# Kernel optimization log

Measured on AMD Instinct MI355X. Metric: run time of the kernel, lower is better.

## Reference

```python
import jax, jax.numpy as jnp
import numpy as np

N = 50000    # num_nodes
E = 800000   # num_edges
IN = 256     # input_dim
H = 256      # hidden_dim
EPS = 1e-5   # BatchNorm eps


def setup_inputs() -> dict:
    key = jax.random.key(0)
    ks = jax.random.split(key, 12)
    def nrm(k, shp, s=0.05):
        return jax.random.normal(k, shp, dtype=jnp.float32) * s
    return {
        "x": jax.random.normal(ks[0], (N, IN), dtype=jnp.float32),
        "edge_index": jax.random.randint(ks[1], (2, E), 0, N, dtype=jnp.int32),
        "edge_weight": jax.random.uniform(ks[2], (E,), dtype=jnp.float32),
        # GCNConv 1 / 2 (PyG stores weight as [in, out]; bias [out])
        "W1": nrm(ks[3], (IN, H)), "b1": jnp.zeros((H,), jnp.float32),
        "W2": nrm(ks[4], (H, H)), "b2": jnp.zeros((H,), jnp.float32),
        # BatchNorm1d 1 / 2
        "gamma1": jnp.ones((H,), jnp.float32), "beta1": jnp.zeros((H,), jnp.float32),
        "gamma2": jnp.ones((H,), jnp.float32), "beta2": jnp.zeros((H,), jnp.float32),
        # LSTM 1 (input 2H) and LSTM 2 (input H), PyTorch gate order i,f,g,o
        "Wih1": nrm(ks[5], (4 * H, 2 * H)), "Whh1": nrm(ks[6], (4 * H, H)),
        "bih1": jnp.zeros((4 * H,), jnp.float32), "bhh1": jnp.zeros((4 * H,), jnp.float32),
        "Wih2": nrm(ks[7], (4 * H, H)), "Whh2": nrm(ks[8], (4 * H, H)),
        "bih2": jnp.zeros((4 * H,), jnp.float32), "bhh2": jnp.zeros((4 * H,), jnp.float32),
    }


def reference(x, edge_index, edge_weight, W1, b1, W2, b2, gamma1, beta1,
              gamma2, beta2, Wih1, Whh1, bih1, bhh1, Wih2, Whh2, bih2, bhh2):
    src, dst = edge_index[0], edge_index[1]
    # GCN symmetric normalization with added self-loops (fill value 1.0)
    loops = jnp.arange(N, dtype=src.dtype)
    src_a = jnp.concatenate([src, loops])
    dst_a = jnp.concatenate([dst, loops])
    ew_a = jnp.concatenate([edge_weight, jnp.ones((N,), edge_weight.dtype)])
    deg = jax.ops.segment_sum(ew_a, dst_a, num_segments=N)
    deg_safe = jnp.where(deg > 0, deg, 1.0)
    dinv = jnp.where(deg > 0, jax.lax.rsqrt(deg_safe), 0.0)
    norm = dinv[src_a] * ew_a * dinv[dst_a]  # [E+N]

    def gcn(h, W, b):
        m = (h @ W)[src_a] * norm[:, None]               # gather + scale messages
        return jax.ops.segment_sum(m, dst_a, num_segments=N) + b

    def bn(h, g, bta):  # training-mode BatchNorm1d (batch stats, biased var)
        mu = jnp.mean(h, axis=0)
        var = jnp.mean((h - mu) ** 2, axis=0)
        return (h - mu) * jax.lax.rsqrt(var + EPS) * g + bta

    def lstm_step0(inp, Wih, bih, bhh):  # single step from h0=c0=0 (window=1)
        gates = inp @ Wih.T + bih + bhh  # Whh term vanishes since h0=0
        i, f, g, o = jnp.split(gates, 4, axis=-1)
        c = jax.nn.sigmoid(i) * jnp.tanh(g)  # f*c0 = 0
        return jax.nn.sigmoid(o) * jnp.tanh(c)

    h1 = bn(jax.nn.relu(gcn(x, W1, b1)), gamma1, beta1)   # [N, H]
    h2 = bn(jax.nn.relu(gcn(h1, W2, b2)), gamma2, beta2)  # [N, H]
    Xc = jnp.concatenate([h1, h2], axis=1)                # [N, 2H]
    hL1 = lstm_step0(Xc, Wih1, bih1, bhh1)                # LSTM1 final hidden
    hL2 = lstm_step0(hL1, Wih2, bih2, bhh2)               # LSTM2 final hidden
    # S with window=1 reduces to x itself
    return jnp.concatenate([hL1, hL2, x], axis=1)         # [N, 2H + IN]
```

## Files before the change

### kernel.cpp

```cpp
#include <hip/hip_runtime.h>
#include <math.h>

#define NN 50000
#define NE 800000

typedef __attribute__((ext_vector_type(8))) short bf8;
typedef __attribute__((ext_vector_type(4))) float f32x4;
typedef unsigned int u32;

__device__ __forceinline__ unsigned short f2b(float f){
  union{float f;unsigned u;} v; v.f=f;
  unsigned r=v.u+0x7fff+((v.u>>16)&1u);
  return (unsigned short)(r>>16);
}
__device__ __forceinline__ float b2f(unsigned short h){
  union{unsigned u;float f;} v; v.u=((unsigned)h)<<16; return v.f;
}
__device__ __forceinline__ float fsigm(float x){ return __builtin_amdgcn_rcpf(1.f+__expf(-x)); }
__device__ __forceinline__ float ftanh(float x){ return 1.f-2.f*__builtin_amdgcn_rcpf(__expf(2.f*x)+1.f); }

__device__ __forceinline__ void gload16(const unsigned short* g, unsigned short* l){
  __builtin_amdgcn_global_load_lds((const __attribute__((address_space(1))) u32*)g,
                                   (__attribute__((address_space(3))) u32*)l,
                                   16,0,0);
}

__global__ __launch_bounds__(256) void k_init(float* deg,int* cnt,float* colsum,float* colsq){
  int i=blockIdx.x*256+threadIdx.x;
  if(i<NN){deg[i]=1.0f;cnt[i]=0;}
  if(i<256){colsum[i]=0.f;colsq[i]=0.f;}
}

__global__ __launch_bounds__(256) void k_deg(const int* __restrict__ ei,const float* __restrict__ ew,
                                             float* deg,int* cnt){
  int e=blockIdx.x*256+threadIdx.x;
  if(e<NE){int d=ei[NE+e];atomicAdd(&deg[d],ew[e]);atomicAdd(&cnt[d],1);}
}

__global__ __launch_bounds__(256) void k_dinv(const float* __restrict__ deg,float* dinv){
  int i=blockIdx.x*256+threadIdx.x;
  if(i<NN){float d=deg[i];dinv[i]=d>0.f?rsqrtf(d):0.f;}
}

__global__ __launch_bounds__(1024) void k_scan(const int* __restrict__ cnt,int* row_ptr,int* cursor){
  __shared__ int s[1024];
  __shared__ int carry;
  int tid=threadIdx.x;
  if(tid==0)carry=0;
  __syncthreads();
  for(int base=0;base<NN;base+=1024){
    int i=base+tid;
    int v=(i<NN)?cnt[i]:0;
    s[tid]=v;__syncthreads();
    for(int off=1;off<1024;off<<=1){
      int t=(tid>=off)?s[tid-off]:0;
      __syncthreads();
      s[tid]+=t;__syncthreads();
    }
    int excl=carry+s[tid]-v;
    if(i<NN){row_ptr[i]=excl;cursor[i]=excl;}
    __syncthreads();
    if(tid==1023)carry+=s[1023];
    __syncthreads();
  }
  if(tid==0)row_ptr[NN]=carry;
}

__global__ __launch_bounds__(256) void k_scatter(const int* __restrict__ ei,const float* __restrict__ ew,
    const float* __restrict__ dinv,int* cursor,int* csr_src,float* csr_w){
  int e=blockIdx.x*256+threadIdx.x;
  if(e<NE){
    int s=ei[e],d=ei[NE+e];
    float wv=dinv[s]*ew[e]*dinv[d];
    int p=atomicAdd(&cursor[d],1);
    csr_src[p]=s;csr_w[p]=wv;
  }
}

__global__ __launch_bounds__(256) void k_wt(const float* __restrict__ W,unsigned short* __restrict__ Wt){
  int j=blockIdx.x,k=threadIdx.x;
  Wt[j*256+k]=f2b(W[k*256+j]);
}
__global__ __launch_bounds__(256) void k_f2b(const float* __restrict__ s,unsigned short* __restrict__ d,int n){
  int i=blockIdx.x*256+threadIdx.x;
  if(i<n)d[i]=f2b(s[i]);
}
__global__ __launch_bounds__(256) void k_cast(const float* __restrict__ s,unsigned short* __restrict__ d){
  long i=(long)blockIdx.x*256+threadIdx.x;
  float4 v=*(const float4*)&s[i*4];
  ushort4 o;o.x=f2b(v.x);o.y=f2b(v.y);o.z=f2b(v.z);o.w=f2b(v.w);
  *(ushort4*)&d[i*4]=o;
}
__global__ __launch_bounds__(256) void k_bsum(const float* __restrict__ a,const float* __restrict__ b,
                                              float* __restrict__ s,int n){
  int i=blockIdx.x*256+threadIdx.x;
  if(i<n)s[i]=a[i]+b[i];
}

__global__ __launch_bounds__(256,2) void k_gemm_mfma(
    const unsigned short* __restrict__ A,int lda,const unsigned short* __restrict__ Bt,int K,
    unsigned short* __restrict__ Cb){
  __shared__ unsigned short As[2][4096];
  __shared__ unsigned short Bs[2][4096];
  int tid=threadIdx.x;
  int row0=blockIdx.x*128,col0=blockIdx.y*128;
  int lane=tid&63,l15=lane&15,quad=lane>>4;
  int wid=tid>>6,wm=wid>>1,wn=wid&1;
  int sr=tid>>2;
  int aoff=((tid&3)^((tid>>3)&3))*8;
  int xq=quad^((l15>>1)&3);
  long ar0=row0+sr;    if(ar0>=NN)ar0=NN-1;
  long ar1=row0+64+sr; if(ar1>=NN)ar1=NN-1;
  const unsigned short* a0p=A+ar0*lda+aoff;
  const unsigned short* a1p=A+ar1*lda+aoff;
  const unsigned short* b0p=Bt+(long)(col0+sr)*K+aoff;
  const unsigned short* b1p=Bt+(long)(col0+64+sr)*K+aoff;
  int lb=wid*512;
  f32x4 acc[4][4]={};
  int nt=K/32;
  gload16(a0p,&As[0][lb]); gload16(a1p,&As[0][2048+lb]);
  gload16(b0p,&Bs[0][lb]); gload16(b1p,&Bs[0][2048+lb]);
  __syncthreads();
  for(int t=0;t<nt;t++){
    int cur=t&1;
    if(t+1<nt){
      int k0=(t+1)*32;int nxt=cur^1;
      gload16(a0p+k0,&As[nxt][lb]); gload16(a1p+k0,&As[nxt][2048+lb]);
      gload16(b0p+k0,&Bs[nxt][lb]); gload16(b1p+k0,&Bs[nxt][2048+lb]);
    }
    bf8 af[4],bfg[4];
    #pragma unroll
    for(int i=0;i<4;i++){
      af[i] =*(const bf8*)&As[cur][(wm*64+i*16+l15)*32+xq*8];
      bfg[i]=*(const bf8*)&Bs[cur][(wn*64+i*16+l15)*32+xq*8];
    }
    #pragma unroll
    for(int mi=0;mi<4;mi++)
      #pragma unroll
      for(int ni=0;ni<4;ni++)
        acc[mi][ni]=__builtin_amdgcn_mfma_f32_16x16x32_bf16(af[mi],bfg[ni],acc[mi][ni],0,0,0);
    __syncthreads();
  }
  #pragma unroll
  for(int mi=0;mi<4;mi++){
    #pragma unroll
    for(int r=0;r<4;r++){
      int node=row0+wm*64+mi*16+quad*4+r;
      if(node>=NN)continue;
      #pragma unroll
      for(int ni=0;ni<4;ni++){
        int col=col0+wn*64+ni*16+l15;
        Cb[(long)node*256+col]=f2b(acc[mi][ni][r]);
      }
    }
  }
}

__global__ __launch_bounds__(256,2) void k_lstm_mfma(
    const unsigned short* __restrict__ A,int lda,int K,
    const unsigned short* __restrict__ Wb,const float* __restrict__ bsum,
    float* __restrict__ Hout,int ldh,unsigned short* __restrict__ Hb){
  __shared__ unsigned short As[2][4096];
  __shared__ unsigned short Bs[2][6144];
  int tid=threadIdx.x;
  int row0=blockIdx.x*128,m0=blockIdx.y*64;
  int lane=tid&63,l15=lane&15,quad=lane>>4;
  int wid=tid>>6,wm=wid>>1,wn=wid&1;
  int sr=tid>>2;
  int aoff=((tid&3)^((tid>>3)&3))*8;
  int xq=quad^((l15>>1)&3);
  long ar0=row0+sr;    if(ar0>=NN)ar0=NN-1;
  long ar1=row0+64+sr; if(ar1>=NN)ar1=NN-1;
  const unsigned short* a0p=A+ar0*lda+aoff;
  const unsigned short* a1p=A+ar1*lda+aoff;
  const unsigned short* wip=Wb+(long)(    m0+sr)*K+aoff;
  const unsigned short* wgp=Wb+(long)(512+m0+sr)*K+aoff;
  const unsigned short* wop=Wb+(long)(768+m0+sr)*K+aoff;
  int lb=wid*512;
  f32x4 ai[4][2]={},ag[4][2]={},ao[4][2]={};
  int nt=K/32;
  gload16(a0p,&As[0][lb]); gload16(a1p,&As[0][2048+lb]);
  gload16(wip,&Bs[0][lb]); gload16(wgp,&Bs[0][2048+lb]); gload16(wop,&Bs[0][4096+lb]);
  __syncthreads();
  for(int t=0;t<nt;t++){
    int cur=t&1;
    if(t+1<nt){
      int k0=(t+1)*32;int nxt=cur^1;
      gload16(a0p+k0,&As[nxt][lb]); gload16(a1p+k0,&As[nxt][2048+lb]);
      gload16(wip+k0,&Bs[nxt][lb]); gload16(wgp+k0,&Bs[nxt][2048+lb]); gload16(wop+k0,&Bs[nxt][4096+lb]);
    }
    bf8 af[4],bi[2],bg[2],bo[2];
    #pragma unroll
    for(int i=0;i<4;i++)af[i]=*(const bf8*)&As[cur][(wm*64+i*16+l15)*32+xq*8];
    #pragma unroll
    for(int ni=0;ni<2;ni++){
      int rr=wn*32+ni*16+l15;
      bi[ni]=*(const bf8*)&Bs[cur][(    rr)*32+xq*8];
      bg[ni]=*(const bf8*)&Bs[cur][( 64+rr)*32+xq*8];
      bo[ni]=*(const bf8*)&Bs[cur][(128+rr)*32+xq*8];
    }
    #pragma unroll
    for(int mi=0;mi<4;mi++)
      #pragma unroll
      for(int ni=0;ni<2;ni++){
        ai[mi][ni]=__builtin_amdgcn_mfma_f32_16x16x32_bf16(af[mi],bi[ni],ai[mi][ni],0,0,0);
        ag[mi][ni]=__builtin_amdgcn_mfma_f32_16x16x32_bf16(af[mi],bg[ni],ag[mi][ni],0,0,0);
        ao[mi][ni]=__builtin_amdgcn_mfma_f32_16x16x32_bf16(af[mi],bo[ni],ao[mi][ni],0,0,0);
      }
    __syncthreads();
  }
  #pragma unroll
  for(int ni=0;ni<2;ni++){
    int m=m0+wn*32+ni*16+l15;
    float b_i=bsum[m],b_g=bsum[512+m],b_o=bsum[768+m];
    #pragma unroll
    for(int mi=0;mi<4;mi++){
      #pragma unroll
      for(int r=0;r<4;r++){
        int node=row0+wm*64+mi*16+quad*4+r;
        if(node>=NN)continue;
        float gi=ai[mi][ni][r]+b_i;
        float gg=ag[mi][ni][r]+b_g;
        float go=ao[mi][ni][r]+b_o;
        float c=fsigm(gi)*ftanh(gg);
        float h=fsigm(go)*ftanh(c);
        Hout[(long)node*ldh+m]=h;
        if(Hb)Hb[(long)node*256+m]=f2b(h);
      }
    }
  }
}

__global__ __launch_bounds__(256) void k_spmm(const unsigned short* __restrict__ Tb,
    const int* __restrict__ row_ptr,const int* __restrict__ csr_src,const float* __restrict__ csr_w,
    const float* __restrict__ dinv,const float* __restrict__ bias,
    unsigned short* __restrict__ Xb,float* colsum,float* colsq){
  __shared__ float s_sum[4][256];
  __shared__ float s_sq[4][256];
  int tid=threadIdx.x;
  int lane=tid&63,wv=tid>>6;
  int c4=lane*4;
  float4 bc=*(const float4*)&bias[c4];
  float sum0=0.f,sum1=0.f,sum2=0.f,sum3=0.f;
  float sq0=0.f,sq1=0.f,sq2=0.f,sq3=0.f;
  int rowbase=blockIdx.x*32+wv*8;
  #pragma unroll 1
  for(int pr=0;pr<4;pr++){
    int ra=rowbase+pr*2,rb=ra+1;
    bool va=ra<NN,vb=rb<NN;
    int raa=va?ra:0,rbb=vb?rb:0;
    int p0a=row_ptr[raa],p1a=row_ptr[raa+1];
    int p0b=row_ptr[rbb],p1b=row_ptr[rbb+1];
    int la=va?(p1a-p0a):0,lb=vb?(p1b-p0b):0;
    float dia=dinv[raa],dib=dinv[rbb];
    ushort4 tsa=*(const ushort4*)&Tb[(long)raa*256+c4];
    ushort4 tsb=*(const ushort4*)&Tb[(long)rbb*256+c4];
    float wsa=dia*dia,wsb=dib*dib;
    float a0=wsa*b2f(tsa.x),a1=wsa*b2f(tsa.y),a2=wsa*b2f(tsa.z),a3=wsa*b2f(tsa.w);
    float b0=wsb*b2f(tsb.x),b1=wsb*b2f(tsb.y),b2=wsb*b2f(tsb.z),b3=wsb*b2f(tsb.w);
    int L=max(la,lb);
    for(int j=0;j<L;j++){
      int ia=j<la?(p0a+j):p0a;
      int ib=j<lb?(p0b+j):p0b;
      float wa=j<la?csr_w[ia]:0.f;
      float wb=j<lb?csr_w[ib]:0.f;
      int sa=csr_src[ia];sa=min(max(sa,0),NN-1);
      int sb=csr_src[ib];sb=min(max(sb,0),NN-1);
      ushort4 ta=*(const ushort4*)&Tb[(long)sa*256+c4];
      ushort4 tb=*(const ushort4*)&Tb[(long)sb*256+c4];
      a0+=wa*b2f(ta.x);a1+=wa*b2f(ta.y);a2+=wa*b2f(ta.z);a3+=wa*b2f(ta.w);
      b0+=wb*b2f(tb.x);b1+=wb*b2f(tb.y);b2+=wb*b2f(tb.z);b3+=wb*b2f(tb.w);
    }
    if(va){
      a0=fmaxf(a0+bc.x,0.f);a1=fmaxf(a1+bc.y,0.f);a2=fmaxf(a2+bc.z,0.f);a3=fmaxf(a3+bc.w,0.f);
      ushort4 o;o.x=f2b(a0);o.y=f2b(a1);o.z=f2b(a2);o.w=f2b(a3);
      *(ushort4*)&Xb[(long)ra*512+c4]=o;
      sum0+=a0;sum1+=a1;sum2+=a2;sum3+=a3;
      sq0+=a0*a0;sq1+=a1*a1;sq2+=a2*a2;sq3+=a3*a3;
    }
    if(vb){
      b0=fmaxf(b0+bc.x,0.f);b1=fmaxf(b1+bc.y,0.f);b2=fmaxf(b2+bc.z,0.f);b3=fmaxf(b3+bc.w,0.f);
      ushort4 o;o.x=f2b(b0);o.y=f2b(b1);o.z=f2b(b2);o.w=f2b(b3);
      *(ushort4*)&Xb[(long)rb*512+c4]=o;
      sum0+=b0;sum1+=b1;sum2+=b2;sum3+=b3;
      sq0+=b0*b0;sq1+=b1*b1;sq2+=b2*b2;sq3+=b3*b3;
    }
  }
  s_sum[wv][c4+0]=sum0;s_sum[wv][c4+1]=sum1;s_sum[wv][c4+2]=sum2;s_sum[wv][c4+3]=sum3;
  s_sq[wv][c4+0]=sq0;s_sq[wv][c4+1]=sq1;s_sq[wv][c4+2]=sq2;s_sq[wv][c4+3]=sq3;
  __syncthreads();
  if(tid<256){
    float a=s_sum[0][tid]+s_sum[1][tid]+s_sum[2][tid]+s_sum[3][tid];
    float q=s_sq[0][tid]+s_sq[1][tid]+s_sq[2][tid]+s_sq[3][tid];
    atomicAdd(&colsum[tid],a);
    atomicAdd(&colsq[tid],q);
  }
}

__global__ __launch_bounds__(256) void k_bnfin(const float* __restrict__ gamma,const float* __restrict__ beta,
    float* colsum,float* colsq,float* scale,float* shift){
  int c=threadIdx.x;
  float mu=colsum[c]/(float)NN;
  float var=colsq[c]/(float)NN-mu*mu;
  float r=rsqrtf(var+1e-5f);
  float sc=r*gamma[c];
  scale[c]=sc;
  shift[c]=beta[c]-mu*sc;
  colsum[c]=0.f;colsq[c]=0.f;
}

__global__ __launch_bounds__(256) void k_bnapply(unsigned short* __restrict__ Xb,
    const float* __restrict__ scale,const float* __restrict__ shift){
  long idx=(long)blockIdx.x*256+threadIdx.x;
  long r=idx>>6;int c=(int)(idx&63)*4;
  if(r<NN){
    ushort4 v=*(const ushort4*)&Xb[r*512+c];
    ushort4 w;
    w.x=f2b(b2f(v.x)*scale[c+0]+shift[c+0]);
    w.y=f2b(b2f(v.y)*scale[c+1]+shift[c+1]);
    w.z=f2b(b2f(v.z)*scale[c+2]+shift[c+2]);
    w.w=f2b(b2f(v.w)*scale[c+3]+shift[c+3]);
    *(ushort4*)&Xb[r*512+c]=w;
  }
}

__global__ __launch_bounds__(256) void k_copy_out(const float* __restrict__ src,
    float* __restrict__ out,int colofs){
  long idx=(long)blockIdx.x*256+threadIdx.x;
  long r=idx>>6;int cc=(int)(idx&63)*4;
  if(r<NN)*(float4*)&out[r*768+colofs+cc]=*(const float4*)&src[r*256+cc];
}

extern "C" void kernel_launch(void* const* d_in,const int* in_sizes,int n_in,
                              void* d_out,int out_size,void* d_ws,size_t ws_size,
                              hipStream_t stream){
  const float* x   =(const float*)d_in[0];
  const int*   ei  =(const int*)  d_in[1];
  const float* ew  =(const float*)d_in[2];
  const float* W1  =(const float*)d_in[3];
  const float* b1  =(const float*)d_in[4];
  const float* W2  =(const float*)d_in[5];
  const float* b2  =(const float*)d_in[6];
  const float* g1  =(const float*)d_in[7];
  const float* be1 =(const float*)d_in[8];
  const float* g2  =(const float*)d_in[9];
  const float* be2 =(const float*)d_in[10];
  const float* Wih1=(const float*)d_in[11];
  const float* bih1=(const float*)d_in[13];
  const float* bhh1=(const float*)d_in[14];
  const float* Wih2=(const float*)d_in[15];
  const float* bih2=(const float*)d_in[17];
  const float* bhh2=(const float*)d_in[18];
  float* out=(float*)d_out;

  char* w=(char*)d_ws;
  auto alloc=[&](size_t bytes)->char*{char* p=w;w+=(bytes+255)&~(size_t)255;return p;};
  float* deg    =(float*)alloc((size_t)NN*4);
  float* dinv   =(float*)alloc((size_t)NN*4);
  int*   cnt    =(int*)  alloc((size_t)NN*4);
  int*   row_ptr=(int*)  alloc((size_t)(NN+1)*4);
  int*   cursor =(int*)  alloc((size_t)NN*4);
  int*   csr_src=(int*)  alloc((size_t)NE*4);
  float* csr_w  =(float*)alloc((size_t)NE*4);
  float* colsum =(float*)alloc(256*4);
  float* colsq  =(float*)alloc(256*4);
  float* scale  =(float*)alloc(256*4);
  float* shift  =(float*)alloc(256*4);
  unsigned short* Xcb =(unsigned short*)alloc((size_t)NN*512*2);
  unsigned short* TbH =(unsigned short*)alloc((size_t)NN*256*2);
  unsigned short* xb  =(unsigned short*)alloc((size_t)NN*256*2);
  unsigned short* Wt1 =(unsigned short*)alloc(256*256*2);
  unsigned short* Wt2 =(unsigned short*)alloc(256*256*2);
  unsigned short* Wb1 =(unsigned short*)alloc((size_t)1024*512*2);
  unsigned short* Wb2 =(unsigned short*)alloc((size_t)1024*256*2);
  float* bs1 =(float*)alloc(1024*4);
  float* bs2 =(float*)alloc(1024*4);

  int nb=(NN+255)/256;
  k_init<<<nb,256,0,stream>>>(deg,cnt,colsum,colsq);
  k_deg<<<(NE+255)/256,256,0,stream>>>(ei,ew,deg,cnt);
  k_dinv<<<nb,256,0,stream>>>(deg,dinv);
  k_scan<<<1,1024,0,stream>>>(cnt,row_ptr,cursor);
  k_scatter<<<(NE+255)/256,256,0,stream>>>(ei,ew,dinv,cursor,csr_src,csr_w);

  k_wt<<<256,256,0,stream>>>(W1,Wt1);
  k_wt<<<256,256,0,stream>>>(W2,Wt2);
  k_cast<<<12500,256,0,stream>>>(x,xb);
  k_f2b<<<(1024*512+255)/256,256,0,stream>>>(Wih1,Wb1,1024*512);
  k_f2b<<<(1024*256+255)/256,256,0,stream>>>(Wih2,Wb2,1024*256);
  k_bsum<<<4,256,0,stream>>>(bih1,bhh1,bs1,1024);
  k_bsum<<<4,256,0,stream>>>(bih2,bhh2,bs2,1024);

  int ngx=(NN+127)/128;
  dim3 gd(ngx,2);
  dim3 gl(ngx,4);
  int nspmm=(NN+31)/32;

  k_gemm_mfma<<<gd,256,0,stream>>>(xb,256,Wt1,256,TbH);
  k_spmm<<<nspmm,256,0,stream>>>(TbH,row_ptr,csr_src,csr_w,dinv,b1,Xcb+0,colsum,colsq);
  k_bnfin<<<1,256,0,stream>>>(g1,be1,colsum,colsq,scale,shift);
  k_bnapply<<<12500,256,0,stream>>>(Xcb+0,scale,shift);
  k_gemm_mfma<<<gd,256,0,stream>>>(Xcb,512,Wt2,256,TbH);
  k_spmm<<<nspmm,256,0,stream>>>(TbH,row_ptr,csr_src,csr_w,dinv,b2,Xcb+256,colsum,colsq);
  k_bnfin<<<1,256,0,stream>>>(g2,be2,colsum,colsq,scale,shift);
  k_bnapply<<<12500,256,0,stream>>>(Xcb+256,scale,shift);
  k_lstm_mfma<<<gl,256,0,stream>>>(Xcb,512,512,Wb1,bs1,out+0,768,TbH);
  k_lstm_mfma<<<gl,256,0,stream>>>(TbH,256,256,Wb2,bs2,out+256,768,nullptr);
  k_copy_out<<<12500,256,0,stream>>>(x,out,512);
}
```

Measured before the change: 863.3 us.

## Fold BatchNorm affine into downstream GEMM weights and widen SpMM row batching

Removes the two BatchNorm apply passes over the 50000x512 activation buffer. The per-column scale is folded into the bf16 GCN2 weights and LSTM1 input weights, and the shift becomes a bias term: a per-column constant times each row's normalized weight sum in SpMM2, and an added bias for LSTM1. The SpMM also now processes four rows per wave at once instead of two pairs sequentially, to expose more memory-level parallelism for the gathers. The cost is extra weight-folding kernels and different rounding, since raw post-ReLU values are stored in bf16 and scaled inside the weights.

```diff
diff --git a/kernel.cpp b/kernel.cpp
--- a/kernel.cpp
+++ b/kernel.cpp
@@ -95,6 +95,37 @@
                                               float* __restrict__ s,int n){
   int i=blockIdx.x*256+threadIdx.x;
   if(i<n)s[i]=a[i]+b[i];
+}
+
+__global__ __launch_bounds__(256) void k_foldw(const float* __restrict__ W,
+    const float* __restrict__ scale,const float* __restrict__ shift,
+    unsigned short* __restrict__ Wt,float* __restrict__ tw){
+  __shared__ float red[256];
+  int j=blockIdx.x,k=threadIdx.x;
+  float w=W[k*256+j];
+  Wt[j*256+k]=f2b(w*scale[k]);
+  red[k]=w*shift[k];
+  __syncthreads();
+  for(int off=128;off>0;off>>=1){ if(k<off)red[k]+=red[k+off]; __syncthreads(); }
+  if(k==0)tw[j]=red[0];
+}
+
+__global__ __launch_bounds__(256) void k_foldlstm(const float* __restrict__ Wih,int K,
+    const float* __restrict__ scale,const float* __restrict__ shift,
+    const float* __restrict__ bih,const float* __restrict__ bhh,
+    unsigned short* __restrict__ Wb,float* __restrict__ bs){
+  __shared__ float red[256];
+  int m=blockIdx.x,t=threadIdx.x;
+  float part=0.f;
+  for(int k=t;k<K;k+=256){
+    float w=Wih[(long)m*K+k];
+    Wb[(long)m*K+k]=f2b(w*scale[k]);
+    part+=w*shift[k];
+  }
+  red[t]=part;
+  __syncthreads();
+  for(int off=128;off>0;off>>=1){ if(t<off)red[t]+=red[t+off]; __syncthreads(); }
+  if(t==0)bs[m]=bih[m]+bhh[m]+red[0];
 }
 
 __global__ __launch_bounds__(256,2) void k_gemm_mfma(
@@ -233,7 +264,7 @@
 
 __global__ __launch_bounds__(256) void k_spmm(const unsigned short* __restrict__ Tb,
     const int* __restrict__ row_ptr,const int* __restrict__ csr_src,const float* __restrict__ csr_w,
-    const float* __restrict__ dinv,const float* __restrict__ bias,
+    const float* __restrict__ dinv,const float* __restrict__ bias,const float* __restrict__ tw,
     unsigned short* __restrict__ Xb,float* colsum,float* colsq){
   __shared__ float s_sum[4][256];
   __shared__ float s_sq[4][256];
@@ -241,50 +272,55 @@
   int lane=tid&63,wv=tid>>6;
   int c4=lane*4;
   float4 bc=*(const float4*)&bias[c4];
+  float4 twc=make_float4(0.f,0.f,0.f,0.f);
+  if(tw)twc=*(const float4*)&tw[c4];
   float sum0=0.f,sum1=0.f,sum2=0.f,sum3=0.f;
   float sq0=0.f,sq1=0.f,sq2=0.f,sq3=0.f;
-  int rowbase=blockIdx.x*32+wv*8;
-  #pragma unroll 1
-  for(int pr=0;pr<4;pr++){
-    int ra=rowbase+pr*2,rb=ra+1;
-    bool va=ra<NN,vb=rb<NN;
-    int raa=va?ra:0,rbb=vb?rb:0;
-    int p0a=row_ptr[raa],p1a=row_ptr[raa+1];
-    int p0b=row_ptr[rbb],p1b=row_ptr[rbb+1];
-    int la=va?(p1a-p0a):0,lb=vb?(p1b-p0b):0;
-    float dia=dinv[raa],dib=dinv[rbb];
-    ushort4 tsa=*(const ushort4*)&Tb[(long)raa*256+c4];
-    ushort4 tsb=*(const ushort4*)&Tb[(long)rbb*256+c4];
-    float wsa=dia*dia,wsb=dib*dib;
-    float a0=wsa*b2f(tsa.x),a1=wsa*b2f(tsa.y),a2=wsa*b2f(tsa.z),a3=wsa*b2f(tsa.w);
-    float b0=wsb*b2f(tsb.x),b1=wsb*b2f(tsb.y),b2=wsb*b2f(tsb.z),b3=wsb*b2f(tsb.w);
-    int L=max(la,lb);
-    for(int j=0;j<L;j++){
-      int ia=j<la?(p0a+j):p0a;
-      int ib=j<lb?(p0b+j):p0b;
-      float wa=j<la?csr_w[ia]:0.f;
-      float wb=j<lb?csr_w[ib]:0.f;
-      int sa=csr_src[ia];sa=min(max(sa,0),NN-1);
-      int sb=csr_src[ib];sb=min(max(sb,0),NN-1);
-      ushort4 ta=*(const ushort4*)&Tb[(long)sa*256+c4];
-      ushort4 tb=*(const ushort4*)&Tb[(long)sb*256+c4];
-      a0+=wa*b2f(ta.x);a1+=wa*b2f(ta.y);a2+=wa*b2f(ta.z);a3+=wa*b2f(ta.w);
-      b0+=wb*b2f(tb.x);b1+=wb*b2f(tb.y);b2+=wb*b2f(tb.z);b3+=wb*b2f(tb.w);
-    }
-    if(va){
-      a0=fmaxf(a0+bc.x,0.f);a1=fmaxf(a1+bc.y,0.f);a2=fmaxf(a2+bc.z,0.f);a3=fmaxf(a3+bc.w,0.f);
-      ushort4 o;o.x=f2b(a0);o.y=f2b(a1);o.z=f2b(a2);o.w=f2b(a3);
-      *(ushort4*)&Xb[(long)ra*512+c4]=o;
-      sum0+=a0;sum1+=a1;sum2+=a2;sum3+=a3;
-      sq0+=a0*a0;sq1+=a1*a1;sq2+=a2*a2;sq3+=a3*a3;
-    }
-    if(vb){
-      b0=fmaxf(b0+bc.x,0.f);b1=fmaxf(b1+bc.y,0.f);b2=fmaxf(b2+bc.z,0.f);b3=fmaxf(b3+bc.w,0.f);
-      ushort4 o;o.x=f2b(b0);o.y=f2b(b1);o.z=f2b(b2);o.w=f2b(b3);
-      *(ushort4*)&Xb[(long)rb*512+c4]=o;
-      sum0+=b0;sum1+=b1;sum2+=b2;sum3+=b3;
-      sq0+=b0*b0;sq1+=b1*b1;sq2+=b2*b2;sq3+=b3*b3;
-    }
+  int rowbase=blockIdx.x*16+wv*4;
+  int rr[4];bool v[4];int p0[4],len[4];
+  float acc[4][4];float rs[4];
+  int Lmax=0;
+  #pragma unroll
+  for(int q=0;q<4;q++){
+    int r=rowbase+q;
+    v[q]=r<NN;
+    int rc=v[q]?r:0;
+    rr[q]=rc;
+    int a=row_ptr[rc],b=row_ptr[rc+1];
+    p0[q]=a;len[q]=v[q]?(b-a):0;
+    Lmax=max(Lmax,len[q]);
+    float di=dinv[rc];float ws=di*di;
+    rs[q]=ws;
+    ushort4 ts=*(const ushort4*)&Tb[(long)rc*256+c4];
+    acc[q][0]=ws*b2f(ts.x);acc[q][1]=ws*b2f(ts.y);acc[q][2]=ws*b2f(ts.z);acc[q][3]=ws*b2f(ts.w);
+  }
+  for(int j=0;j<Lmax;j++){
+    int idx[4];float wq[4];int sidx[4];
+    #pragma unroll
+    for(int q=0;q<4;q++){
+      idx[q]=(j<len[q])?(p0[q]+j):p0[q];
+      wq[q]=(j<len[q])?csr_w[idx[q]]:0.f;
+      int s=csr_src[idx[q]];sidx[q]=min(max(s,0),NN-1);
+    }
+    #pragma unroll
+    for(int q=0;q<4;q++){
+      ushort4 t=*(const ushort4*)&Tb[(long)sidx[q]*256+c4];
+      acc[q][0]+=wq[q]*b2f(t.x);acc[q][1]+=wq[q]*b2f(t.y);
+      acc[q][2]+=wq[q]*b2f(t.z);acc[q][3]+=wq[q]*b2f(t.w);
+      rs[q]+=wq[q];
+    }
+  }
+  #pragma unroll
+  for(int q=0;q<4;q++){
+    if(!v[q])continue;
+    float a0=fmaxf(acc[q][0]+rs[q]*twc.x+bc.x,0.f);
+    float a1=fmaxf(acc[q][1]+rs[q]*twc.y+bc.y,0.f);
+    float a2=fmaxf(acc[q][2]+rs[q]*twc.z+bc.z,0.f);
+    float a3=fmaxf(acc[q][3]+rs[q]*twc.w+bc.w,0.f);
+    ushort4 o;o.x=f2b(a0);o.y=f2b(a1);o.z=f2b(a2);o.w=f2b(a3);
+    *(ushort4*)&Xb[(long)rr[q]*512+c4]=o;
+    sum0+=a0;sum1+=a1;sum2+=a2;sum3+=a3;
+    sq0+=a0*a0;sq1+=a1*a1;sq2+=a2*a2;sq3+=a3*a3;
   }
   s_sum[wv][c4+0]=sum0;s_sum[wv][c4+1]=sum1;s_sum[wv][c4+2]=sum2;s_sum[wv][c4+3]=sum3;
   s_sq[wv][c4+0]=sq0;s_sq[wv][c4+1]=sq1;s_sq[wv][c4+2]=sq2;s_sq[wv][c4+3]=sq3;
@@ -307,21 +343,6 @@
   scale[c]=sc;
   shift[c]=beta[c]-mu*sc;
   colsum[c]=0.f;colsq[c]=0.f;
-}
-
-__global__ __launch_bounds__(256) void k_bnapply(unsigned short* __restrict__ Xb,
-    const float* __restrict__ scale,const float* __restrict__ shift){
-  long idx=(long)blockIdx.x*256+threadIdx.x;
-  long r=idx>>6;int c=(int)(idx&63)*4;
-  if(r<NN){
-    ushort4 v=*(const ushort4*)&Xb[r*512+c];
-    ushort4 w;
-    w.x=f2b(b2f(v.x)*scale[c+0]+shift[c+0]);
-    w.y=f2b(b2f(v.y)*scale[c+1]+shift[c+1]);
-    w.z=f2b(b2f(v.z)*scale[c+2]+shift[c+2]);
-    w.w=f2b(b2f(v.w)*scale[c+3]+shift[c+3]);
-    *(ushort4*)&Xb[r*512+c]=w;
-  }
 }
 
 __global__ __launch_bounds__(256) void k_copy_out(const float* __restrict__ src,
@@ -364,8 +385,9 @@
   float* csr_w  =(float*)alloc((size_t)NE*4);
   float* colsum =(float*)alloc(256*4);
   float* colsq  =(float*)alloc(256*4);
-  float* scale  =(float*)alloc(256*4);
-  float* shift  =(float*)alloc(256*4);
+  float* scale  =(float*)alloc(512*4);
+  float* shift  =(float*)alloc(512*4);
+  float* tw     =(float*)alloc(256*4);
   unsigned short* Xcb =(unsigned short*)alloc((size_t)NN*512*2);
   unsigned short* TbH =(unsigned short*)alloc((size_t)NN*256*2);
   unsigned short* xb  =(unsigned short*)alloc((size_t)NN*256*2);
@@ -384,26 +406,23 @@
   k_scatter<<<(NE+255)/256,256,0,stream>>>(ei,ew,dinv,cursor,csr_src,csr_w);
 
   k_wt<<<256,256,0,stream>>>(W1,Wt1);
-  k_wt<<<256,256,0,stream>>>(W2,Wt2);
   k_cast<<<12500,256,0,stream>>>(x,xb);
-  k_f2b<<<(1024*512+255)/256,256,0,stream>>>(Wih1,Wb1,1024*512);
   k_f2b<<<(1024*256+255)/256,256,0,stream>>>(Wih2,Wb2,1024*256);
-  k_bsum<<<4,256,0,stream>>>(bih1,bhh1,bs1,1024);
   k_bsum<<<4,256,0,stream>>>(bih2,bhh2,bs2,1024);
 
   int ngx=(NN+127)/128;
   dim3 gd(ngx,2);
   dim3 gl(ngx,4);
-  int nspmm=(NN+31)/32;
+  int nspmm=(NN+15)/16;
 
   k_gemm_mfma<<<gd,256,0,stream>>>(xb,256,Wt1,256,TbH);
-  k_spmm<<<nspmm,256,0,stream>>>(TbH,row_ptr,csr_src,csr_w,dinv,b1,Xcb+0,colsum,colsq);
+  k_spmm<<<nspmm,256,0,stream>>>(TbH,row_ptr,csr_src,csr_w,dinv,b1,nullptr,Xcb+0,colsum,colsq);
   k_bnfin<<<1,256,0,stream>>>(g1,be1,colsum,colsq,scale,shift);
-  k_bnapply<<<12500,256,0,stream>>>(Xcb+0,scale,shift);
+  k_foldw<<<256,256,0,stream>>>(W2,scale,shift,Wt2,tw);
   k_gemm_mfma<<<gd,256,0,stream>>>(Xcb,512,Wt2,256,TbH);
-  k_spmm<<<nspmm,256,0,stream>>>(TbH,row_ptr,csr_src,csr_w,dinv,b2,Xcb+256,colsum,colsq);
-  k_bnfin<<<1,256,0,stream>>>(g2,be2,colsum,colsq,scale,shift);
-  k_bnapply<<<12500,256,0,stream>>>(Xcb+256,scale,shift);
+  k_spmm<<<nspmm,256,0,stream>>>(TbH,row_ptr,csr_src,csr_w,dinv,b2,tw,Xcb+256,colsum,colsq);
+  k_bnfin<<<1,256,0,stream>>>(g2,be2,colsum,colsq,scale+256,shift+256);
+  k_foldlstm<<<1024,256,0,stream>>>(Wih1,512,scale,shift,bih1,bhh1,Wb1,bs1);
   k_lstm_mfma<<<gl,256,0,stream>>>(Xcb,512,512,Wb1,bs1,out+0,768,TbH);
   k_lstm_mfma<<<gl,256,0,stream>>>(TbH,256,256,Wb2,bs2,out+256,768,nullptr);
   k_copy_out<<<12500,256,0,stream>>>(x,out,512);
```

New measurement: 881.9 us. 1.02x slower.
